# Performance work log

Hardware: AMD Instinct MI355X
Metric: run time of the kernel (lower is better)

Reference implementation:

```python
import jax, jax.numpy as jnp
import numpy as np

SLOPE = 0.2
NEG = -9e15

def setup_inputs() -> dict:
    key = jax.random.key(0)
    k1, k2, k3, k4 = jax.random.split(key, 4)
    N, INP, OUT = 8192, 512, 128
    h = jax.random.normal(k1, (N, INP), dtype=jnp.float32)
    adj = jax.random.randint(k2, (N, N), 0, 2, dtype=jnp.int32)
    W = jax.random.normal(k3, (INP, OUT), dtype=jnp.float32) * (1.0 / np.sqrt(INP))
    a = jax.random.normal(k4, (2 * OUT,), dtype=jnp.float32) * (1.0 / np.sqrt(2 * OUT))
    return {"h": h, "adj": adj, "W": W, "a": a}

def reference(h, adj, W, a):
    OUT = W.shape[1]
    Wh = h @ W                               # [N, out]
    # a . [Wh_i, Wh_j] decomposes into two matvecs (same math as pairwise concat)
    f1 = Wh @ a[:OUT]                        # [N]
    f2 = Wh @ a[OUT:]                        # [N]
    e = jax.nn.leaky_relu(f1[:, None] + f2[None, :], negative_slope=SLOPE)  # [N, N]
    scores = jnp.where(adj > 0, e, NEG)
    attention = jax.nn.softmax(scores, axis=1)
    return attention @ Wh                    # [N, out]
```

## Files before the change

### kernel.cpp

```cpp
#include <hip/hip_runtime.h>

typedef unsigned short u16;
typedef unsigned int u32;
typedef __attribute__((ext_vector_type(8))) short short8v;
typedef __attribute__((ext_vector_type(4))) float float4v;
typedef __attribute__((ext_vector_type(4))) int   int4v;

#define N_NODES 8192
#define D_IN    512
#define D_OUT   128
#define SLOPEF  0.2f
#define LOG2E   1.4426950408889634f
#define NSEG    4
#define SEGCOLS 2048
#define NCHUNK  8

static __device__ __forceinline__ u16 f2bf(float f) {
    union { float f; unsigned int i; } v; v.f = f;
    unsigned int r = v.i + 0x7fff + ((v.i >> 16) & 1);
    return (u16)(r >> 16);
}
static __device__ __forceinline__ void lds_barrier() {
    asm volatile("s_waitcnt lgkmcnt(0)" ::: "memory");
    __builtin_amdgcn_s_barrier();
    asm volatile("" ::: "memory");
}

__global__ __launch_bounds__(256) void kb_pack(
        const int* __restrict__ adj, unsigned long long* __restrict__ mask64)
{
    const int lane = threadIdx.x & 63;
    const int gw = (blockIdx.x * 256 + threadIdx.x) >> 6;
    #pragma unroll
    for (int it = 0; it < 8; ++it) {
        const int* base = adj + ((size_t)gw * 64 + it * 8) * 64 + lane;
        int v[8];
        #pragma unroll
        for (int g = 0; g < 8; g++) v[g] = base[g * 64];
        unsigned long long b[8];
        #pragma unroll
        for (int g = 0; g < 8; g++) b[g] = __ballot(v[g] > 0);
        unsigned long long myb = b[0];
        #pragma unroll
        for (int g = 1; g < 8; g++) myb = (lane == g) ? b[g] : myb;
        if (lane < 8) mask64[(size_t)gw * 64 + it * 8 + lane] = myb;
    }
}

__global__ __launch_bounds__(256, 2) void k1_proj(
        const float* __restrict__ h, const float* __restrict__ W,
        const float* __restrict__ a, u16* __restrict__ WhT,
        float* __restrict__ f1, float* __restrict__ f2)
{
    __shared__ float hs[16 * D_IN];
    __shared__ float buf[16 * 128];
    __shared__ float part[16][17];
    const int tid = threadIdx.x;
    const int rowbase = blockIdx.x * 16;

    const float4v* hsrc = (const float4v*)(h + (size_t)rowbase * D_IN);
    #pragma unroll
    for (int i = 0; i < 8; i++) {
        *(float4v*)&hs[(tid + 256 * i) * 4] = hsrc[tid + 256 * i];
    }
    __syncthreads();

    const int c  = tid & 127;
    const int rh = tid >> 7;
    float acc[8];
    #pragma unroll
    for (int rr = 0; rr < 8; rr++) acc[rr] = 0.f;

    for (int k = 0; k < D_IN; k += 4) {
        float wv[4];
        #pragma unroll
        for (int kk = 0; kk < 4; kk++) wv[kk] = W[(k + kk) * D_OUT + c];
        #pragma unroll
        for (int rr = 0; rr < 8; rr++) {
            float4v hv = *(const float4v*)&hs[(rh * 8 + rr) * D_IN + k];
            acc[rr] += hv[0] * wv[0];
            acc[rr] += hv[1] * wv[1];
            acc[rr] += hv[2] * wv[2];
            acc[rr] += hv[3] * wv[3];
        }
    }

    {
        short8v pack;
        #pragma unroll
        for (int rr = 0; rr < 8; rr++) pack[rr] = (short)f2bf(acc[rr]);
        *(short8v*)(WhT + (size_t)c * N_NODES + rowbase + rh * 8) = pack;
    }

    const float a1 = a[c];
    const float a2 = a[D_OUT + c];

    #pragma unroll
    for (int rr = 0; rr < 8; rr++) buf[(rh * 8 + rr) * 128 + c] = acc[rr] * a1;
    __syncthreads();
    {
        const int row = tid >> 4, seg = tid & 15;
        float p = 0.f;
        #pragma unroll
        for (int e = 0; e < 8; e++) p += buf[row * 128 + seg * 8 + e];
        part[row][seg] = p;
    }
    __syncthreads();
    if (tid < 16) {
        float s = 0.f;
        #pragma unroll
        for (int j = 0; j < 16; j++) s += part[tid][j];
        f1[rowbase + tid] = s * LOG2E;
    }
    __syncthreads();
    #pragma unroll
    for (int rr = 0; rr < 8; rr++) buf[(rh * 8 + rr) * 128 + c] = acc[rr] * a2;
    __syncthreads();
    {
        const int row = tid >> 4, seg = tid & 15;
        float p = 0.f;
        #pragma unroll
        for (int e = 0; e < 8; e++) p += buf[row * 128 + seg * 8 + e];
        part[row][seg] = p;
    }
    __syncthreads();
    if (tid < 16) {
        float s = 0.f;
        #pragma unroll
        for (int j = 0; j < 16; j++) s += part[tid][j];
        f2[rowbase + tid] = s * LOG2E;
    }
}

__global__ __launch_bounds__(256, 4) void k2_attn(
        const u32* __restrict__ mask, const u16* __restrict__ WhT,
        const float* __restrict__ f1g, const float* __restrict__ f2g,
        float* __restrict__ numw, float* __restrict__ denw)
{
    __shared__ short Pt[32 * 264];
    __shared__ float f2s[2304];
    __shared__ float f1s[32];
    __shared__ float rs[32][9];
    __shared__ float ssum[32];

    const int tid = threadIdx.x;
    const int rb  = blockIdx.x >> 2;
    const int seg = blockIdx.x & 3;
    const int rowbase = rb * 32;
    const int colbase = seg * SEGCOLS;
    const int r = tid >> 3, g = tid & 7;
    const int lane = tid & 63, w = tid >> 6;
    const int quad = lane >> 4, m16 = lane & 15;

    if (tid < 32) f1s[tid] = f1g[rowbase + tid];
    #pragma unroll
    for (int i = 0; i < 2; i++) {
        const int idx = (tid + 256 * i) * 4;
        *(float4v*)&f2s[idx + ((idx >> 5) << 2)] = *(const float4v*)&f2g[colbase + idx];
    }

    const u32* mrow = mask + (size_t)(rowbase + r) * (N_NODES / 32) + seg * (SEGCOLS / 32);
    u32 mcur = mrow[g];

    float4v acc[2][2];
    #pragma unroll
    for (int mt = 0; mt < 2; mt++)
        #pragma unroll
        for (int nt = 0; nt < 2; nt++) {
            acc[mt][nt][0] = 0.f; acc[mt][nt][1] = 0.f;
            acc[mt][nt][2] = 0.f; acc[mt][nt][3] = 0.f;
        }
    float ls0 = 0.f, ls1 = 0.f, ls2 = 0.f, ls3 = 0.f;

    __syncthreads();

    for (int jc = 0; jc < NCHUNK; jc++) {
        u32 mnext = 0;
        if (jc + 1 < NCHUNK) mnext = mrow[(jc + 1) * 8 + g];

        const float f1v = f1s[r];
        const float* f2p = &f2s[jc * 288 + g * 36];
        u32 packed[16];
        #pragma unroll
        for (int i = 0; i < 8; i++) {
            const float4v fv = *(const float4v*)&f2p[i * 4];
            u32 wb[4];
            #pragma unroll
            for (int e = 0; e < 4; e++) {
                const int idx = i * 4 + e;
                const int sel = ((int)(mcur << (31 - idx))) >> 31;
                float x = f1v + fv[e];
                x = fmaxf(x, SLOPEF * x);
                const float ex = __builtin_amdgcn_exp2f(x);
                const u32 wt = __float_as_uint(ex) & ((u32)sel & 0xffff0000u);
                wb[e] = wt;
                if (e == 0) ls0 += __uint_as_float(wt);
                else if (e == 1) ls1 += __uint_as_float(wt);
                else if (e == 2) ls2 += __uint_as_float(wt);
                else ls3 += __uint_as_float(wt);
            }
            packed[i * 2]     = __builtin_amdgcn_perm(wb[1], wb[0], 0x07060302);
            packed[i * 2 + 1] = __builtin_amdgcn_perm(wb[3], wb[2], 0x07060302);
        }
        {
            int* pdst = (int*)&Pt[r * 264 + g * 32];
            #pragma unroll
            for (int q = 0; q < 4; q++) {
                int4v st;
                st[0] = (int)packed[q * 4 + 0]; st[1] = (int)packed[q * 4 + 1];
                st[2] = (int)packed[q * 4 + 2]; st[3] = (int)packed[q * 4 + 3];
                *(int4v*)&pdst[q * 4] = st;
            }
        }
        mcur = mnext;
        lds_barrier();

        {
            const u16* b0p = WhT + (size_t)(w * 32 + m16) * N_NODES + colbase + jc * 256 + quad * 8;
            const u16* b1p = b0p + 16 * N_NODES;
            const short* a0p = &Pt[m16 * 264 + quad * 8];
            const short* a1p = a0p + 16 * 264;
            #pragma unroll
            for (int ks = 0; ks < 8; ks++) {
                const int ko = ks * 32;
                const short8v af0 = *(const short8v*)(a0p + ko);
                const short8v af1 = *(const short8v*)(a1p + ko);
                const short8v bv0 = *(const short8v*)(b0p + ko);
                const short8v bv1 = *(const short8v*)(b1p + ko);
                acc[0][0] = __builtin_amdgcn_mfma_f32_16x16x32_bf16(af0, bv0, acc[0][0], 0, 0, 0);
                acc[0][1] = __builtin_amdgcn_mfma_f32_16x16x32_bf16(af0, bv1, acc[0][1], 0, 0, 0);
                acc[1][0] = __builtin_amdgcn_mfma_f32_16x16x32_bf16(af1, bv0, acc[1][0], 0, 0, 0);
                acc[1][1] = __builtin_amdgcn_mfma_f32_16x16x32_bf16(af1, bv1, acc[1][1], 0, 0, 0);
            }
        }
        lds_barrier();
    }

    rs[r][g] = (ls0 + ls1) + (ls2 + ls3);
    __syncthreads();
    if (tid < 32) {
        float s = 0.f;
        #pragma unroll
        for (int j = 0; j < 8; j++) s += rs[tid][j];
        ssum[tid] = s;
        denw[(size_t)(rowbase + tid) * NSEG + seg] = s;
    }
    __syncthreads();

    #pragma unroll
    for (int mt = 0; mt < 2; mt++) {
        #pragma unroll
        for (int nt = 0; nt < 2; nt++) {
            const int cl = w * 32 + nt * 16 + m16;
            #pragma unroll
            for (int reg = 0; reg < 4; reg++) {
                const int rl = mt * 16 + quad * 4 + reg;
                numw[((size_t)(rowbase + rl) * NSEG + seg) * D_OUT + cl] = acc[mt][nt][reg];
            }
        }
    }
}

__global__ __launch_bounds__(256) void k3_reduce(
        const float* __restrict__ numw, const float* __restrict__ denw,
        float* __restrict__ out)
{
    const int tid = threadIdx.x;
    const int row = blockIdx.x * 2 + (tid >> 7);
    const int c   = tid & 127;
    float s = 0.f, d = 0.f;
    #pragma unroll
    for (int sg = 0; sg < NSEG; sg++) {
        s += numw[((size_t)row * NSEG + sg) * D_OUT + c];
        d += denw[(size_t)row * NSEG + sg];
    }
    out[(size_t)row * D_OUT + c] = s / d;
}

extern "C" void kernel_launch(void* const* d_in, const int* in_sizes, int n_in,
                              void* d_out, int out_size, void* d_ws, size_t ws_size,
                              hipStream_t stream) {
    const float* h   = (const float*)d_in[0];
    const int*   adj = (const int*)d_in[1];
    const float* W   = (const float*)d_in[2];
    const float* a   = (const float*)d_in[3];

    char* ws = (char*)d_ws;
    unsigned long long* mask64 = (unsigned long long*)ws;
    u16*   WhT = (u16*)(ws + (size_t)8 * 1024 * 1024);
    float* f1  = (float*)(ws + (size_t)10 * 1024 * 1024);
    float* f2  = f1 + N_NODES;
    float* numw = (float*)(ws + (size_t)12 * 1024 * 1024);
    float* denw = (float*)(ws + (size_t)28 * 1024 * 1024);

    kb_pack<<<4096, 256, 0, stream>>>(adj, mask64);
    k1_proj<<<N_NODES / 16, 256, 0, stream>>>(h, W, a, WhT, f1, f2);
    k2_attn<<<(N_NODES / 32) * NSEG, 256, 0, stream>>>((const u32*)mask64, WhT, f1, f2, numw, denw);
    k3_reduce<<<N_NODES / 2, 256, 0, stream>>>(numw, denw, (float*)d_out);
}
```

Measured before the change: 474.7 us.

## Read int adjacency directly in attention kernel and use bf16 MFMA for projection

Drops the separate adjacency bit-packing kernel; the attention kernel now loads int32 adjacency rows directly and builds the mask inline, prefetching the next chunk into registers. This removes one full pass over the 256MB adjacency matrix plus a launch, at the cost of 32x more mask bytes read inside the attention kernel and higher register pressure. The fp32 scalar projection is replaced by a conversion kernel (h and W to bf16, W transposed) followed by an MFMA-based projection with 32-row tiles. The projection therefore runs at lower precision.

```diff
diff --git a/kernel.cpp b/kernel.cpp
--- a/kernel.cpp
+++ b/kernel.cpp
@@ -3,6 +3,7 @@
 typedef unsigned short u16;
 typedef unsigned int u32;
 typedef __attribute__((ext_vector_type(8))) short short8v;
+typedef __attribute__((ext_vector_type(4))) short short4v;
 typedef __attribute__((ext_vector_type(4))) float float4v;
 typedef __attribute__((ext_vector_type(4))) int   int4v;
 
@@ -26,114 +27,133 @@
     asm volatile("" ::: "memory");
 }
 
-__global__ __launch_bounds__(256) void kb_pack(
-        const int* __restrict__ adj, unsigned long long* __restrict__ mask64)
+__global__ __launch_bounds__(256) void kc_convert(
+        const float* __restrict__ h, const float* __restrict__ W,
+        u16* __restrict__ hb, u16* __restrict__ WbT)
 {
-    const int lane = threadIdx.x & 63;
-    const int gw = (blockIdx.x * 256 + threadIdx.x) >> 6;
-    #pragma unroll
-    for (int it = 0; it < 8; ++it) {
-        const int* base = adj + ((size_t)gw * 64 + it * 8) * 64 + lane;
-        int v[8];
-        #pragma unroll
-        for (int g = 0; g < 8; g++) v[g] = base[g * 64];
-        unsigned long long b[8];
-        #pragma unroll
-        for (int g = 0; g < 8; g++) b[g] = __ballot(v[g] > 0);
-        unsigned long long myb = b[0];
-        #pragma unroll
-        for (int g = 1; g < 8; g++) myb = (lane == g) ? b[g] : myb;
-        if (lane < 8) mask64[(size_t)gw * 64 + it * 8 + lane] = myb;
-    }
-}
-
-__global__ __launch_bounds__(256, 2) void k1_proj(
-        const float* __restrict__ h, const float* __restrict__ W,
+    if (blockIdx.x < 2048) {
+        const size_t t = (size_t)blockIdx.x * 256 + threadIdx.x;
+        const float4v* src = (const float4v*)h + t * 2;
+        const float4v v0 = src[0], v1 = src[1];
+        short8v o;
+        o[0] = (short)f2bf(v0[0]); o[1] = (short)f2bf(v0[1]);
+        o[2] = (short)f2bf(v0[2]); o[3] = (short)f2bf(v0[3]);
+        o[4] = (short)f2bf(v1[0]); o[5] = (short)f2bf(v1[1]);
+        o[6] = (short)f2bf(v1[2]); o[7] = (short)f2bf(v1[3]);
+        *(short8v*)(hb + t * 8) = o;
+    } else {
+        const int t2 = (blockIdx.x - 2048) * 256 + threadIdx.x;
+        const int k = t2 >> 4;
+        const int n0 = (t2 & 15) * 8;
+        const float4v* src = (const float4v*)(W + (size_t)k * D_OUT + n0);
+        const float4v v0 = src[0], v1 = src[1];
+        #pragma unroll
+        for (int e = 0; e < 4; e++) WbT[(size_t)(n0 + e) * D_IN + k] = f2bf(v0[e]);
+        #pragma unroll
+        for (int e = 0; e < 4; e++) WbT[(size_t)(n0 + 4 + e) * D_IN + k] = f2bf(v1[e]);
+    }
+}
+
+__global__ __launch_bounds__(256) void k1m_proj(
+        const u16* __restrict__ hb, const u16* __restrict__ WbT,
         const float* __restrict__ a, u16* __restrict__ WhT,
         float* __restrict__ f1, float* __restrict__ f2)
 {
-    __shared__ float hs[16 * D_IN];
-    __shared__ float buf[16 * 128];
-    __shared__ float part[16][17];
+    __shared__ short As[32 * 136];
+    __shared__ short Ws[128 * 136];
+    __shared__ float pf1[32][65];
+    __shared__ float pf2[32][65];
+
     const int tid = threadIdx.x;
-    const int rowbase = blockIdx.x * 16;
-
-    const float4v* hsrc = (const float4v*)(h + (size_t)rowbase * D_IN);
-    #pragma unroll
-    for (int i = 0; i < 8; i++) {
-        *(float4v*)&hs[(tid + 256 * i) * 4] = hsrc[tid + 256 * i];
-    }
+    const int rowbase = blockIdx.x * 32;
+    const int lane = tid & 63, w = tid >> 6;
+    const int quad = lane >> 4, m16 = lane & 15;
+
+    float4v acc[2][2];
+    #pragma unroll
+    for (int mt = 0; mt < 2; mt++)
+        #pragma unroll
+        for (int nt = 0; nt < 2; nt++) {
+            acc[mt][nt][0] = 0.f; acc[mt][nt][1] = 0.f;
+            acc[mt][nt][2] = 0.f; acc[mt][nt][3] = 0.f;
+        }
+
+    for (int c = 0; c < 4; c++) {
+        const int kc0 = c * 128;
+        if (c) __syncthreads();
+        {
+            const int row = tid >> 3, koff = (tid & 7) * 16;
+            const short8v* src = (const short8v*)(hb + (size_t)(rowbase + row) * D_IN + kc0 + koff);
+            const short8v s0 = src[0], s1 = src[1];
+            *(short8v*)&As[row * 136 + koff] = s0;
+            *(short8v*)&As[row * 136 + koff + 8] = s1;
+        }
+        {
+            const int n = tid & 127, h2 = tid >> 7;
+            #pragma unroll
+            for (int i = 0; i < 8; i++) {
+                const int koff = h2 * 64 + i * 8;
+                *(short8v*)&Ws[n * 136 + koff] =
+                    *(const short8v*)(WbT + (size_t)n * D_IN + kc0 + koff);
+            }
+        }
+        __syncthreads();
+        #pragma unroll
+        for (int ks = 0; ks < 4; ks++) {
+            const int ko = ks * 32 + quad * 8;
+            const short8v af0 = *(const short8v*)&As[m16 * 136 + ko];
+            const short8v af1 = *(const short8v*)&As[(16 + m16) * 136 + ko];
+            const short8v bf0 = *(const short8v*)&Ws[(w * 32 + m16) * 136 + ko];
+            const short8v bf1 = *(const short8v*)&Ws[(w * 32 + 16 + m16) * 136 + ko];
+            acc[0][0] = __builtin_amdgcn_mfma_f32_16x16x32_bf16(af0, bf0, acc[0][0], 0, 0, 0);
+            acc[0][1] = __builtin_amdgcn_mfma_f32_16x16x32_bf16(af0, bf1, acc[0][1], 0, 0, 0);
+            acc[1][0] = __builtin_amdgcn_mfma_f32_16x16x32_bf16(af1, bf0, acc[1][0], 0, 0, 0);
+            acc[1][1] = __builtin_amdgcn_mfma_f32_16x16x32_bf16(af1, bf1, acc[1][1], 0, 0, 0);
+        }
+    }
+
+    #pragma unroll
+    for (int mt = 0; mt < 2; mt++) {
+        #pragma unroll
+        for (int nt = 0; nt < 2; nt++) {
+            const int n = w * 32 + nt * 16 + m16;
+            short4v p;
+            #pragma unroll
+            for (int reg = 0; reg < 4; reg++) p[reg] = (short)f2bf(acc[mt][nt][reg]);
+            *(short4v*)(WhT + (size_t)n * N_NODES + rowbase + mt * 16 + quad * 4) = p;
+        }
+    }
+
+    float a1v[2], a2v[2];
+    #pragma unroll
+    for (int nt = 0; nt < 2; nt++) {
+        a1v[nt] = a[w * 32 + nt * 16 + m16];
+        a2v[nt] = a[D_OUT + w * 32 + nt * 16 + m16];
+    }
+    #pragma unroll
+    for (int mt = 0; mt < 2; mt++)
+        #pragma unroll
+        for (int reg = 0; reg < 4; reg++) {
+            const int row = mt * 16 + quad * 4 + reg;
+            pf1[row][w * 16 + m16] = acc[mt][0][reg] * a1v[0] + acc[mt][1][reg] * a1v[1];
+            pf2[row][w * 16 + m16] = acc[mt][0][reg] * a2v[0] + acc[mt][1][reg] * a2v[1];
+        }
     __syncthreads();
-
-    const int c  = tid & 127;
-    const int rh = tid >> 7;
-    float acc[8];
-    #pragma unroll
-    for (int rr = 0; rr < 8; rr++) acc[rr] = 0.f;
-
-    for (int k = 0; k < D_IN; k += 4) {
-        float wv[4];
-        #pragma unroll
-        for (int kk = 0; kk < 4; kk++) wv[kk] = W[(k + kk) * D_OUT + c];
-        #pragma unroll
-        for (int rr = 0; rr < 8; rr++) {
-            float4v hv = *(const float4v*)&hs[(rh * 8 + rr) * D_IN + k];
-            acc[rr] += hv[0] * wv[0];
-            acc[rr] += hv[1] * wv[1];
-            acc[rr] += hv[2] * wv[2];
-            acc[rr] += hv[3] * wv[3];
-        }
-    }
-
-    {
-        short8v pack;
-        #pragma unroll
-        for (int rr = 0; rr < 8; rr++) pack[rr] = (short)f2bf(acc[rr]);
-        *(short8v*)(WhT + (size_t)c * N_NODES + rowbase + rh * 8) = pack;
-    }
-
-    const float a1 = a[c];
-    const float a2 = a[D_OUT + c];
-
-    #pragma unroll
-    for (int rr = 0; rr < 8; rr++) buf[(rh * 8 + rr) * 128 + c] = acc[rr] * a1;
-    __syncthreads();
-    {
-        const int row = tid >> 4, seg = tid & 15;
-        float p = 0.f;
-        #pragma unroll
-        for (int e = 0; e < 8; e++) p += buf[row * 128 + seg * 8 + e];
-        part[row][seg] = p;
-    }
-    __syncthreads();
-    if (tid < 16) {
+    if (tid < 32) {
         float s = 0.f;
         #pragma unroll
-        for (int j = 0; j < 16; j++) s += part[tid][j];
+        for (int j = 0; j < 64; j++) s += pf1[tid][j];
         f1[rowbase + tid] = s * LOG2E;
-    }
-    __syncthreads();
-    #pragma unroll
-    for (int rr = 0; rr < 8; rr++) buf[(rh * 8 + rr) * 128 + c] = acc[rr] * a2;
-    __syncthreads();
-    {
-        const int row = tid >> 4, seg = tid & 15;
-        float p = 0.f;
-        #pragma unroll
-        for (int e = 0; e < 8; e++) p += buf[row * 128 + seg * 8 + e];
-        part[row][seg] = p;
-    }
-    __syncthreads();
-    if (tid < 16) {
+    } else if (tid < 64) {
         float s = 0.f;
         #pragma unroll
-        for (int j = 0; j < 16; j++) s += part[tid][j];
-        f2[rowbase + tid] = s * LOG2E;
+        for (int j = 0; j < 64; j++) s += pf2[tid - 32][j];
+        f2[rowbase + tid - 32] = s * LOG2E;
     }
 }
 
 __global__ __launch_bounds__(256, 4) void k2_attn(
-        const u32* __restrict__ mask, const u16* __restrict__ WhT,
+        const int* __restrict__ adj, const u16* __restrict__ WhT,
         const float* __restrict__ f1g, const float* __restrict__ f2g,
         float* __restrict__ numw, float* __restrict__ denw)
 {
@@ -159,8 +179,10 @@
         *(float4v*)&f2s[idx + ((idx >> 5) << 2)] = *(const float4v*)&f2g[colbase + idx];
     }
 
-    const u32* mrow = mask + (size_t)(rowbase + r) * (N_NODES / 32) + seg * (SEGCOLS / 32);
-    u32 mcur = mrow[g];
+    const int4v* arow = (const int4v*)(adj + (size_t)(rowbase + r) * N_NODES + colbase);
+    int4v a4[8];
+    #pragma unroll
+    for (int i = 0; i < 8; i++) a4[i] = arow[g * 8 + i];
 
     float4v acc[2][2];
     #pragma unroll
@@ -175,24 +197,21 @@
     __syncthreads();
 
     for (int jc = 0; jc < NCHUNK; jc++) {
-        u32 mnext = 0;
-        if (jc + 1 < NCHUNK) mnext = mrow[(jc + 1) * 8 + g];
-
         const float f1v = f1s[r];
         const float* f2p = &f2s[jc * 288 + g * 36];
         u32 packed[16];
         #pragma unroll
         for (int i = 0; i < 8; i++) {
             const float4v fv = *(const float4v*)&f2p[i * 4];
+            const int4v av = a4[i];
             u32 wb[4];
             #pragma unroll
             for (int e = 0; e < 4; e++) {
-                const int idx = i * 4 + e;
-                const int sel = ((int)(mcur << (31 - idx))) >> 31;
+                const u32 msk = (av[e] > 0) ? 0xffff0000u : 0u;
                 float x = f1v + fv[e];
                 x = fmaxf(x, SLOPEF * x);
                 const float ex = __builtin_amdgcn_exp2f(x);
-                const u32 wt = __float_as_uint(ex) & ((u32)sel & 0xffff0000u);
+                const u32 wt = __float_as_uint(ex) & msk;
                 wb[e] = wt;
                 if (e == 0) ls0 += __uint_as_float(wt);
                 else if (e == 1) ls1 += __uint_as_float(wt);
@@ -212,7 +231,10 @@
                 *(int4v*)&pdst[q * 4] = st;
             }
         }
-        mcur = mnext;
+        if (jc + 1 < NCHUNK) {
+            #pragma unroll
+            for (int i = 0; i < 8; i++) a4[i] = arow[(jc + 1) * 64 + g * 8 + i];
+        }
         lds_barrier();
 
         {
@@ -286,15 +308,16 @@
     const float* a   = (const float*)d_in[3];
 
     char* ws = (char*)d_ws;
-    unsigned long long* mask64 = (unsigned long long*)ws;
-    u16*   WhT = (u16*)(ws + (size_t)8 * 1024 * 1024);
-    float* f1  = (float*)(ws + (size_t)10 * 1024 * 1024);
-    float* f2  = f1 + N_NODES;
+    u16*   hb   = (u16*)ws;
+    u16*   WbT  = (u16*)(ws + (size_t)8 * 1024 * 1024);
+    u16*   WhT  = (u16*)(ws + (size_t)9 * 1024 * 1024);
+    float* f1   = (float*)(ws + (size_t)11 * 1024 * 1024);
+    float* f2   = f1 + N_NODES;
     float* numw = (float*)(ws + (size_t)12 * 1024 * 1024);
     float* denw = (float*)(ws + (size_t)28 * 1024 * 1024);
 
-    kb_pack<<<4096, 256, 0, stream>>>(adj, mask64);
-    k1_proj<<<N_NODES / 16, 256, 0, stream>>>(h, W, a, WhT, f1, f2);
-    k2_attn<<<(N_NODES / 32) * NSEG, 256, 0, stream>>>((const u32*)mask64, WhT, f1, f2, numw, denw);
+    kc_convert<<<2080, 256, 0, stream>>>(h, W, hb, WbT);
+    k1m_proj<<<N_NODES / 32, 256, 0, stream>>>(hb, WbT, a, WhT, f1, f2);
+    k2_attn<<<(N_NODES / 32) * NSEG, 256, 0, stream>>>(adj, WhT, f1, f2, numw, denw);
     k3_reduce<<<N_NODES / 2, 256, 0, stream>>>(numw, denw, (float*)d_out);
 }
```

Result: faster. 420.1 us (-11.5%).
